# Kernel optimization log

Measured on AMD Instinct MI355X. Metric: run time of the kernel, lower is better.

The kernel has to match this reference:

```python
import jax, jax.numpy as jnp
import numpy as np

CONST = 0.0  # init kwarg `const`


def setup_inputs() -> dict:
    key = jax.random.key(0)
    kx, = jax.random.split(key, 1)
    B, C, H, W = 16, 1, 2048, 2048
    x = jax.random.normal(kx, (B, C, H, W), dtype=jnp.float32)
    a = jnp.ones((3,), dtype=jnp.float32)   # stencil params: center, horiz, vert
    w = jnp.ones((4,), dtype=jnp.float32)   # polynomial coeffs w0..w3 (poly_order=3)
    return {"x": x, "a": a, "w": w}


def reference(x, a, w):
    # Replicate-pad H and W by 1 (== F.pad(x, (1,1,1,1), 'replicate'))
    xp = jnp.pad(x, ((0, 0), (0, 0), (1, 1), (1, 1)), mode="edge")
    # 5-point stencil conv: kernel center=a0, left/right=a1, up/down=a2, corners=0.
    # Expressed as shifted adds instead of a dense conv (same math, one memory pass).
    center = x
    horiz = xp[:, :, 1:-1, :-2] + xp[:, :, 1:-1, 2:]   # left + right neighbors
    vert = xp[:, :, :-2, 1:-1] + xp[:, :, 2:, 1:-1]    # up + down neighbors
    stencil = a[0] * center + a[1] * horiz + a[2] * vert
    # Polynomial p = w0 + w1*d + w2*d^2 + w3*d^3 with d = x - const (Horner form)
    d = x - CONST
    p = w[3]
    p = p * d + w[2]
    p = p * d + w[1]
    p = p * d + w[0]
    return stencil + p
```

## Files before the change

kernel.cpp:

```cpp
#include <hip/hip_runtime.h>


#define H_DIM 2048
#define W_DIM 2048
#define W4    (W_DIM / 4)

__global__ __launch_bounds__(256) void FCNN_63651415326860_kernel(
    const float* __restrict__ x,
    const float* __restrict__ a,
    const float* __restrict__ w,
    float* __restrict__ out)
{
    const int v = blockIdx.x * blockDim.x + threadIdx.x;
    const int col4 = v & (W4 - 1);
    const int rowg = v >> 9;
    const int row  = rowg & (H_DIM - 1);

    const float4* x4 = (const float4*)x;

    const float4 c  = x4[v];
    const float4 up = (row == 0)         ? c : x4[v - W4];
    const float4 dn = (row == H_DIM - 1) ? c : x4[v + W4];

    const float leftN  = (col4 == 0)      ? c.x : x[(size_t)v * 4 - 1];
    const float rightN = (col4 == W4 - 1) ? c.w : x[(size_t)v * 4 + 4];

    const float a0 = a[0], a1 = a[1], a2 = a[2];
    const float w0 = w[0], w1 = w[1], w2 = w[2], w3 = w[3];

    float4 r;
    {
        const float h  = leftN + c.y;
        const float vv = up.x + dn.x;
        const float s  = a0 * c.x + a1 * h + a2 * vv;
        const float p  = fmaf(fmaf(fmaf(w3, c.x, w2), c.x, w1), c.x, w0);
        r.x = s + p;
    }
    {
        const float h  = c.x + c.z;
        const float vv = up.y + dn.y;
        const float s  = a0 * c.y + a1 * h + a2 * vv;
        const float p  = fmaf(fmaf(fmaf(w3, c.y, w2), c.y, w1), c.y, w0);
        r.y = s + p;
    }
    {
        const float h  = c.y + c.w;
        const float vv = up.z + dn.z;
        const float s  = a0 * c.z + a1 * h + a2 * vv;
        const float p  = fmaf(fmaf(fmaf(w3, c.z, w2), c.z, w1), c.z, w0);
        r.z = s + p;
    }
    {
        const float h  = c.z + rightN;
        const float vv = up.w + dn.w;
        const float s  = a0 * c.w + a1 * h + a2 * vv;
        const float p  = fmaf(fmaf(fmaf(w3, c.w, w2), c.w, w1), c.w, w0);
        r.w = s + p;
    }

    ((float4*)out)[v] = r;
}

extern "C" void kernel_launch(void* const* d_in, const int* in_sizes, int n_in,
                              void* d_out, int out_size, void* d_ws, size_t ws_size,
                              hipStream_t stream) {
    const float* x = (const float*)d_in[0];
    const float* a = (const float*)d_in[1];
    const float* w = (const float*)d_in[2];
    float* out = (float*)d_out;

    const int total4 = out_size / 4;
    const int block = 256;
    const int grid = total4 / block;

    FCNN_63651415326860_kernel<<<grid, block, 0, stream>>>(x, a, w, out);
}
```

Measured before the change: 505.2 us.

## Process eight rows per thread with register row reuse and shuffled halos

Each thread now sweeps down eight rows of a column group, carrying the centre and up rows in registers so each input row is loaded once. Left and right neighbours are obtained via wave shuffles, with global loads only at wave edges. Output uses nontemporal stores and block indices are swizzled across bands. This aims to cut redundant global/cache traffic, at the cost of fewer blocks and a serial load dependency per thread.

```diff
diff --git a/kernel.cpp b/kernel.cpp
--- a/kernel.cpp
+++ b/kernel.cpp
@@ -4,61 +4,67 @@
 #define H_DIM 2048
 #define W_DIM 2048
 #define W4    (W_DIM / 4)
+#define RPT   8
+#define BLK   256
 
-__global__ __launch_bounds__(256) void FCNN_63651415326860_kernel(
+typedef float fvec4 __attribute__((ext_vector_type(4)));
+
+__global__ __launch_bounds__(BLK) void FCNN_63651415326860_kernel(
     const float* __restrict__ x,
     const float* __restrict__ a,
     const float* __restrict__ w,
     float* __restrict__ out)
 {
-    const int v = blockIdx.x * blockDim.x + threadIdx.x;
-    const int col4 = v & (W4 - 1);
-    const int rowg = v >> 9;
-    const int row  = rowg & (H_DIM - 1);
+    const int chunk = gridDim.x >> 3;
+    const int swz   = (blockIdx.x & 7) * chunk + (blockIdx.x >> 3);
 
-    const float4* x4 = (const float4*)x;
+    const int half = swz & 1;
+    const int band = swz >> 1;
 
-    const float4 c  = x4[v];
-    const float4 up = (row == 0)         ? c : x4[v - W4];
-    const float4 dn = (row == H_DIM - 1) ? c : x4[v + W4];
+    const int col4 = half * BLK + (int)threadIdx.x;
+    const int lane = threadIdx.x & 63;
 
-    const float leftN  = (col4 == 0)      ? c.x : x[(size_t)v * 4 - 1];
-    const float rightN = (col4 == W4 - 1) ? c.w : x[(size_t)v * 4 + 4];
+    const int rowg0 = band * RPT;
+    const int row0  = rowg0 & (H_DIM - 1);
+
+    const float4* __restrict__ x4 = (const float4*)x;
 
     const float a0 = a[0], a1 = a[1], a2 = a[2];
     const float w0 = w[0], w1 = w[1], w2 = w[2], w3 = w[3];
 
-    float4 r;
-    {
-        const float h  = leftN + c.y;
-        const float vv = up.x + dn.x;
-        const float s  = a0 * c.x + a1 * h + a2 * vv;
-        const float p  = fmaf(fmaf(fmaf(w3, c.x, w2), c.x, w1), c.x, w0);
-        r.x = s + p;
+    int v = rowg0 * W4 + col4;
+
+    float4 cur = x4[v];
+    float4 up  = (row0 == 0) ? cur : x4[v - W4];
+
+    #pragma unroll
+    for (int r = 0; r < RPT; ++r) {
+        const int row = row0 + r;
+        const float4 dn = (row == H_DIM - 1) ? cur : x4[v + W4];
+
+        float lw = __shfl(cur.w, (lane > 0)  ? lane - 1 : 0);
+        float rw = __shfl(cur.x, (lane < 63) ? lane + 1 : 63);
+        if (lane == 0)
+            lw = (col4 == 0)      ? cur.x : x[(size_t)v * 4 - 1];
+        if (lane == 63)
+            rw = (col4 == W4 - 1) ? cur.w : x[(size_t)v * 4 + 4];
+
+        fvec4 res;
+        res.x = a0 * cur.x + a1 * (lw    + cur.y) + a2 * (up.x + dn.x)
+              + fmaf(fmaf(fmaf(w3, cur.x, w2), cur.x, w1), cur.x, w0);
+        res.y = a0 * cur.y + a1 * (cur.x + cur.z) + a2 * (up.y + dn.y)
+              + fmaf(fmaf(fmaf(w3, cur.y, w2), cur.y, w1), cur.y, w0);
+        res.z = a0 * cur.z + a1 * (cur.y + cur.w) + a2 * (up.z + dn.z)
+              + fmaf(fmaf(fmaf(w3, cur.z, w2), cur.z, w1), cur.z, w0);
+        res.w = a0 * cur.w + a1 * (cur.z + rw   ) + a2 * (up.w + dn.w)
+              + fmaf(fmaf(fmaf(w3, cur.w, w2), cur.w, w1), cur.w, w0);
+
+        __builtin_nontemporal_store(res, (fvec4*)(out + (size_t)v * 4));
+
+        up = cur;
+        cur = dn;
+        v += W4;
     }
-    {
-        const float h  = c.x + c.z;
-        const float vv = up.y + dn.y;
-        const float s  = a0 * c.y + a1 * h + a2 * vv;
-        const float p  = fmaf(fmaf(fmaf(w3, c.y, w2), c.y, w1), c.y, w0);
-        r.y = s + p;
-    }
-    {
-        const float h  = c.y + c.w;
-        const float vv = up.z + dn.z;
-        const float s  = a0 * c.z + a1 * h + a2 * vv;
-        const float p  = fmaf(fmaf(fmaf(w3, c.z, w2), c.z, w1), c.z, w0);
-        r.z = s + p;
-    }
-    {
-        const float h  = c.z + rightN;
-        const float vv = up.w + dn.w;
-        const float s  = a0 * c.w + a1 * h + a2 * vv;
-        const float p  = fmaf(fmaf(fmaf(w3, c.w, w2), c.w, w1), c.w, w0);
-        r.w = s + p;
-    }
-
-    ((float4*)out)[v] = r;
 }
 
 extern "C" void kernel_launch(void* const* d_in, const int* in_sizes, int n_in,
@@ -70,8 +76,7 @@
     float* out = (float*)d_out;
 
     const int total4 = out_size / 4;
-    const int block = 256;
-    const int grid = total4 / block;
+    const int grid = total4 / (BLK * RPT);
 
-    FCNN_63651415326860_kernel<<<grid, block, 0, stream>>>(x, a, w, out);
+    FCNN_63651415326860_kernel<<<grid, BLK, 0, stream>>>(x, a, w, out);
 }
```

New measurement: 456.8 us. -9.6%, faster.
